# Kernel optimization log

Measured on AMD Instinct MI355X. Metric: run time of the kernel, lower is better.

## Reference

```python
import jax, jax.numpy as jnp
import numpy as np

NV, B, E, H, LF = 32, 32768, 16, 4, 4
D = E // H
FF = LF * E
EPS = 1e-5


def _gelu(x):
    return jax.nn.gelu(x, approximate=False)


def _ln(x, g, b):
    m = x.mean(-1, keepdims=True)
    v = ((x - m) ** 2).mean(-1, keepdims=True)
    return (x - m) * jax.lax.rsqrt(v + EPS) * g + b


def _mha(q_in, kv_in, wi, bi, wo, bo):
    # torch nn.MultiheadAttention, seq-first layout (S, B, E), eval mode (no dropout)
    wq, wk, wv = jnp.split(wi, 3, axis=0)
    bq, bk, bv = jnp.split(bi, 3)
    Sq, Bn = q_in.shape[0], q_in.shape[1]
    Sk = kv_in.shape[0]
    q = (q_in @ wq.T + bq).reshape(Sq, Bn, H, D)
    k = (kv_in @ wk.T + bk).reshape(Sk, Bn, H, D)
    v = (kv_in @ wv.T + bv).reshape(Sk, Bn, H, D)
    s = jnp.einsum('qbhd,kbhd->bhqk', q, k) / jnp.sqrt(jnp.asarray(D, q.dtype))
    a = jax.nn.softmax(s, axis=-1)
    o = jnp.einsum('bhqk,kbhd->qbhd', a, v).reshape(Sq, Bn, E)
    return o @ wo.T + bo


def setup_inputs() -> dict:
    key = jax.random.key(0)
    ks = iter(jax.random.split(key, 32))
    r = lambda *shape: 0.1 * jax.random.normal(next(ks), shape, dtype=jnp.float32)
    return {
        'x': jax.random.normal(next(ks), (B, NV), dtype=jnp.float32),
        'emb_w1': r(NV, LF), 'emb_b1': r(NV, LF),            # per-feature Linear(1, LF)
        'emb_w2': r(NV, LF, E), 'emb_b2': r(NV, E),          # per-feature Linear(LF, E)
        'ln1_g': jnp.ones((E,), jnp.float32), 'ln1_b': jnp.zeros((E,), jnp.float32),
        'attn_wi': r(3 * E, E), 'attn_bi': r(3 * E),
        'attn_wo': r(E, E), 'attn_bo': r(E),
        'ln2_g': jnp.ones((E,), jnp.float32), 'ln2_b': jnp.zeros((E,), jnp.float32),
        'fc1_w': r(FF, E), 'fc1_b': r(FF),
        'fc2_w': r(E, FF), 'fc2_b': r(E),
        'cls_token': jnp.zeros((E,), jnp.float32),
        'cln1_g': jnp.ones((E,), jnp.float32), 'cln1_b': jnp.zeros((E,), jnp.float32),
        'cattn_wi': r(3 * E, E), 'cattn_bi': r(3 * E),
        'cattn_wo': r(E, E), 'cattn_bo': r(E),
        'cln2_g': jnp.ones((E,), jnp.float32), 'cln2_b': jnp.zeros((E,), jnp.float32),
        'clsfc_w': r(1, E), 'clsfc_b': r(1),
    }


def reference(x, emb_w1, emb_b1, emb_w2, emb_b2, ln1_g, ln1_b,
              attn_wi, attn_bi, attn_wo, attn_bo, ln2_g, ln2_b,
              fc1_w, fc1_b, fc2_w, fc2_b, cls_token,
              cln1_g, cln1_b, cattn_wi, cattn_bi, cattn_wo, cattn_bo,
              cln2_g, cln2_b, clsfc_w, clsfc_b):
    # --- per-feature tokenizer: batched tiny MLPs (vectorized over nvars) ---
    h = _gelu(x[:, :, None] * emb_w1[None] + emb_b1[None])          # (B, NV, LF)
    e = _gelu(jnp.einsum('bvf,vfe->bve', h, emb_w2) + emb_b2[None]) # (B, NV, E)
    t = jnp.transpose(e, (1, 0, 2))                                 # (NV, B, E) seq-first
    # --- encoder block (pre-norm) ---
    res = t
    t = _ln(t, ln1_g, ln1_b)
    t = _mha(t, t, attn_wi, attn_bi, attn_wo, attn_bo) + res
    res = t
    t = _ln(t, ln2_g, ln2_b)
    t = _gelu(t @ fc1_w.T + fc1_b) @ fc2_w.T + fc2_b
    t = t + res
    # --- class-token decoder ---
    cls = jnp.broadcast_to(cls_token, (1, t.shape[1], E))           # (1, B, E)
    u = jnp.concatenate([cls, t], axis=0)                           # (NV+1, B, E)
    un = _ln(u, cln1_g, cln1_b)
    c = _mha(cls, un, cattn_wi, cattn_bi, cattn_wo, cattn_bo) + cls # query is raw cls
    c = _ln(c, cln2_g, cln2_b)
    c = c[0]                                                        # (B, E)
    out = jax.nn.sigmoid(c @ clsfc_w.T + clsfc_b)                   # (B, 1)
    return out
```

## Files before the change

### kernel.cpp

```cpp
#include <hip/hip_runtime.h>
#include <hip/hip_bf16.h>
#include <math.h>

#define NV 32
#define E  16
#define FF 64
#define BATCH 32768
#define L2E 1.4426950408889634f

static constexpr float EPS = 1e-5f;

typedef __attribute__((ext_vector_type(8)))  short bf16x8;
typedef __attribute__((ext_vector_type(16))) float f32x16;
typedef __attribute__((ext_vector_type(4)))  unsigned u32x4;

__device__ __forceinline__ short f2bf(float f) {
    __hip_bfloat16 h = __float2bfloat16(f);
    return __builtin_bit_cast(short, h);
}
__device__ __forceinline__ unsigned pack2(float a, float b) {
    return (unsigned)(unsigned short)f2bf(a) | ((unsigned)(unsigned short)f2bf(b) << 16);
}
__device__ __forceinline__ void halfswap(unsigned &a, unsigned &b) {
    const auto r = __builtin_amdgcn_permlane32_swap(a, b, false, false);
    a = (unsigned)r[0]; b = (unsigned)r[1];
}
__device__ __forceinline__ float addxhalf(float v) {
    const unsigned u = __builtin_bit_cast(unsigned, v);
    const auto r = __builtin_amdgcn_permlane32_swap(u, u, false, false);
    return __builtin_bit_cast(float, (unsigned)r[0]) + __builtin_bit_cast(float, (unsigned)r[1]);
}
__device__ __forceinline__ int psi(int h, int i) {
    return 4 * h + (i & 3) + 8 * (i >> 2);
}
__device__ __forceinline__ float ex2(float x) { return __builtin_amdgcn_exp2f(x); }
__device__ __forceinline__ float gelu_fast(float x) {
    const float x2 = x * x;
    const float u  = x * fmaf(x2, 0.10294324f, 2.3022082f);
    return x - x * __builtin_amdgcn_rcpf(1.0f + ex2(u));
}
__device__ __forceinline__ bf16x8 pack8(const float* v) {
    bf16x8 r;
#pragma unroll
    for (int i = 0; i < 8; i++) r[i] = f2bf(v[i]);
    return r;
}
__device__ __forceinline__ float dot16(const float* __restrict__ wrow, const float* __restrict__ v) {
    float s = 0.f;
#pragma unroll
    for (int j = 0; j < 16; j++) s = fmaf(wrow[j], v[j], s);
    return s;
}

__global__ __launch_bounds__(256, 4) void event_classifier_kernel(
    const float* __restrict__ x,
    const float* __restrict__ emb_w1,
    const float* __restrict__ emb_b1,
    const float* __restrict__ emb_w2,
    const float* __restrict__ emb_b2,
    const float* __restrict__ ln1_g, const float* __restrict__ ln1_b,
    const float* __restrict__ attn_wi,
    const float* __restrict__ attn_bi,
    const float* __restrict__ attn_wo,
    const float* __restrict__ attn_bo,
    const float* __restrict__ ln2_g, const float* __restrict__ ln2_b,
    const float* __restrict__ fc1_w,
    const float* __restrict__ fc1_b,
    const float* __restrict__ fc2_w,
    const float* __restrict__ fc2_b,
    const float* __restrict__ cls_token,
    const float* __restrict__ cln1_g, const float* __restrict__ cln1_b,
    const float* __restrict__ cattn_wi,
    const float* __restrict__ cattn_bi,
    const float* __restrict__ cattn_wo,
    const float* __restrict__ cattn_bo,
    const float* __restrict__ cln2_g, const float* __restrict__ cln2_b,
    const float* __restrict__ clsfc_w,
    const float* __restrict__ clsfc_b,
    float* __restrict__ out)
{
    __shared__ alignas(16) unsigned s_frag[11][64][4];
    __shared__ alignas(16) float s_bias[8][32];
    __shared__ alignas(16) unsigned short s_vt[4][4][5][40];
    __shared__ alignas(16) float s_cls[48];
    __shared__ alignas(16) float s_cw[20];

    const int tid = threadIdx.x;
    const int l   = tid & 63;
    const int t   = l & 31;
    const int hh  = l >> 5;
    const int w   = tid >> 6;
    const int b   = blockIdx.x * 4 + w;

    for (int f0 = 0; f0 < 12; f0 += 4) {
        const int f = f0 + w;
        if (f < 11) {
            const float* W; const float* gc = nullptr;
            int stride = 16, coff = 0; bool valid = true; float rscale = 1.0f;
            switch (f) {
                case 0:  W = attn_wi;        gc = ln1_g; if (t < 16) rscale = 0.5f * L2E; break;
                case 1:  W = attn_wi + 512;  gc = ln1_g; valid = (t < 16); break;
                case 2:  W = attn_wo;        valid = (t < 16); break;
                case 3:  W = fc1_w;          gc = ln2_g; break;
                case 4:  W = fc1_w + 512;    gc = ln2_g; break;
                case 5: case 6: case 7: case 8:
                         W = fc2_w; stride = 64; coff = (f - 5) * 16; valid = (t < 16); break;
                case 9:  W = cattn_wi + 256; gc = cln1_g; break;
                default: W = cattn_wo;       valid = (t < 16); break;
            }
            unsigned d[4] = {0u, 0u, 0u, 0u};
            if (valid) {
                const float* row = W + t * stride + coff;
#pragma unroll
                for (int e2 = 0; e2 < 4; e2++) {
                    const int p0 = psi(hh, 2 * e2), p1 = psi(hh, 2 * e2 + 1);
                    const float g0 = gc ? gc[p0] : 1.0f;
                    const float g1 = gc ? gc[p1] : 1.0f;
                    d[e2] = pack2(row[p0] * g0 * rscale, row[p1] * g1 * rscale);
                }
            }
            s_frag[f][l][0] = d[0]; s_frag[f][l][1] = d[1];
            s_frag[f][l][2] = d[2]; s_frag[f][l][3] = d[3];
        }
    }
    {
        const int i = tid;
        const int mat = i >> 5, idx = i & 31, h2 = idx >> 4, r = idx & 15;
        const int p8 = psi(h2, r & 7);
        float val = 0.f;
        switch (mat) {
            case 0:
                if (r < 8) val = (attn_bi[p8] + dot16(attn_wi + p8 * 16, ln1_b)) * (0.5f * L2E);
                else       val =  attn_bi[16 + p8] + dot16(attn_wi + (16 + p8) * 16, ln1_b);
                break;
            case 1: if (r < 8) val = attn_bi[32 + p8] + dot16(attn_wi + (32 + p8) * 16, ln1_b); break;
            case 2: if (r < 8) val = attn_bo[p8]; break;
            case 3: { const int p16 = psi(h2, r); val = fc1_b[p16] + dot16(fc1_w + p16 * 16, ln2_b); } break;
            case 4: { const int p16 = psi(h2, r); val = fc1_b[32 + p16] + dot16(fc1_w + (32 + p16) * 16, ln2_b); } break;
            case 5: if (r < 8) val = fc2_b[p8]; break;
            case 6:
                if (r < 8) val = cattn_bi[16 + p8] + dot16(cattn_wi + (16 + p8) * 16, cln1_b);
                else       val = cattn_bi[32 + p8] + dot16(cattn_wi + (32 + p8) * 16, cln1_b);
                break;
            default: if (r < 8) val = cattn_bo[p8] + cls_token[p8]; break;
        }
        s_bias[mat][idx] = val;
    }
    if (tid < 16) {
        const int jp = tid;
        float cls[E];
        float m = 0.f;
#pragma unroll
        for (int j = 0; j < E; j++) { cls[j] = cls_token[j]; m += cls[j]; }
        m *= (1.0f / E);
        float var = 0.f;
#pragma unroll
        for (int j = 0; j < E; j++) { float d = cls[j] - m; var += d * d; }
        var *= (1.0f / E);
        float r = rsqrtf(var + EPS);
        float un0[E];
#pragma unroll
        for (int j = 0; j < E; j++) un0[j] = (cls[j] - m) * r * cln1_g[j] + cln1_b[j];
        float qq = cattn_bi[jp], kk = cattn_bi[16 + jp], vv2 = cattn_bi[32 + jp];
#pragma unroll
        for (int j = 0; j < E; j++) {
            qq  += cls[j] * cattn_wi[jp * E + j];
            kk  += un0[j] * cattn_wi[(16 + jp) * E + j];
            vv2 += un0[j] * cattn_wi[(32 + jp) * E + j];
        }
        s_cls[jp] = qq * (0.5f * L2E); s_cls[16 + jp] = kk; s_cls[32 + jp] = vv2;
        s_cw[jp] = cln2_g[jp] * clsfc_w[jp];
        if (jp == 0) {
            float s = clsfc_b[0];
#pragma unroll
            for (int j = 0; j < E; j++) s = fmaf(cln2_b[j], clsfc_w[j], s);
            s_cw[16] = s;
        }
    }
    __syncthreads();

#define LD4(p) (*reinterpret_cast<const float4*>(p))
#define FRAG(f) (*reinterpret_cast<const bf16x8*>(&s_frag[f][l][0]))
#define CBIAS8(mat, c) { const float4 lo_ = LD4(&s_bias[mat][hh*16]); \
                         const float4 hi_ = LD4(&s_bias[mat][hh*16+4]); \
                         c[0]=lo_.x; c[1]=lo_.y; c[2]=lo_.z; c[3]=lo_.w; \
                         c[4]=hi_.x; c[5]=hi_.y; c[6]=hi_.z; c[7]=hi_.w; \
                         c[8]=0;c[9]=0;c[10]=0;c[11]=0;c[12]=0;c[13]=0;c[14]=0;c[15]=0; }
#define CBIAS16(mat, c) { const float4 a_ = LD4(&s_bias[mat][hh*16]); \
                          const float4 b_ = LD4(&s_bias[mat][hh*16+4]); \
                          const float4 c_ = LD4(&s_bias[mat][hh*16+8]); \
                          const float4 d_ = LD4(&s_bias[mat][hh*16+12]); \
                          c[0]=a_.x;c[1]=a_.y;c[2]=a_.z;c[3]=a_.w; \
                          c[4]=b_.x;c[5]=b_.y;c[6]=b_.z;c[7]=b_.w; \
                          c[8]=c_.x;c[9]=c_.y;c[10]=c_.z;c[11]=c_.w; \
                          c[12]=d_.x;c[13]=d_.y;c[14]=d_.z;c[15]=d_.w; }

    f32x16 z16;
#pragma unroll
    for (int i = 0; i < 16; i++) z16[i] = 0.0f;

    const float xv = x[b * NV + t];
    float F[8];
    {
        const float4 w1 = LD4(emb_w1 + t * 4);
        const float4 b1 = LD4(emb_b1 + t * 4);
        float hb[4];
        hb[0] = gelu_fast(fmaf(xv, w1.x, b1.x));
        hb[1] = gelu_fast(fmaf(xv, w1.y, b1.y));
        hb[2] = gelu_fast(fmaf(xv, w1.z, b1.z));
        hb[3] = gelu_fast(fmaf(xv, w1.w, b1.w));
        float a[8];
        const float4 bA = LD4(emb_b2 + t * 16 + 4 * hh);
        const float4 bB = LD4(emb_b2 + t * 16 + 8 + 4 * hh);
        a[0]=bA.x; a[1]=bA.y; a[2]=bA.z; a[3]=bA.w;
        a[4]=bB.x; a[5]=bB.y; a[6]=bB.z; a[7]=bB.w;
#pragma unroll
        for (int f = 0; f < 4; f++) {
            const float4 wA = LD4(emb_w2 + t * 64 + f * 16 + 4 * hh);
            const float4 wB = LD4(emb_w2 + t * 64 + f * 16 + 8 + 4 * hh);
            a[0] = fmaf(hb[f], wA.x, a[0]); a[1] = fmaf(hb[f], wA.y, a[1]);
            a[2] = fmaf(hb[f], wA.z, a[2]); a[3] = fmaf(hb[f], wA.w, a[3]);
            a[4] = fmaf(hb[f], wB.x, a[4]); a[5] = fmaf(hb[f], wB.y, a[5]);
            a[6] = fmaf(hb[f], wB.z, a[6]); a[7] = fmaf(hb[f], wB.w, a[7]);
        }
#pragma unroll
        for (int r = 0; r < 8; r++) F[r] = gelu_fast(a[r]);
    }

#define LN_CANON(src, dst) { \
        float s_ = 0.f; \
        _Pragma("unroll") for (int r = 0; r < 8; r++) s_ += src[r]; \
        s_ = addxhalf(s_); \
        const float m_ = s_ * (1.0f / 16.0f); \
        float vs_ = 0.f; \
        _Pragma("unroll") for (int r = 0; r < 8; r++) { float d_ = src[r] - m_; vs_ = fmaf(d_, d_, vs_); } \
        vs_ = addxhalf(vs_); \
        const float rs_ = rsqrtf(vs_ * (1.0f / 16.0f) + EPS); \
        _Pragma("unroll") for (int r = 0; r < 8; r++) dst[r] = (src[r] - m_) * rs_; }

    float res[8];
#pragma unroll
    for (int r = 0; r < 8; r++) res[r] = F[r];
    float tn[8];
    LN_CANON(F, tn);

    const bf16x8 bt = pack8(tn);
    f32x16 cqk, cv;
    CBIAS16(0, cqk); CBIAS8(1, cv);
    const f32x16 dqk = __builtin_amdgcn_mfma_f32_32x32x16_bf16(FRAG(0), bt, cqk, 0, 0, 0);
    const f32x16 dv  = __builtin_amdgcn_mfma_f32_32x32x16_bf16(FRAG(1), bt, cv, 0, 0, 0);

    unsigned qx0 = pack2(dqk[0],  dqk[1]),  qx1 = pack2(dqk[2],  dqk[3]);
    unsigned qx2 = pack2(dqk[4],  dqk[5]),  qx3 = pack2(dqk[6],  dqk[7]);
    unsigned kx0 = pack2(dqk[8],  dqk[9]),  kx1 = pack2(dqk[10], dqk[11]);
    unsigned kx2 = pack2(dqk[12], dqk[13]), kx3 = pack2(dqk[14], dqk[15]);
    halfswap(qx0, qx1); halfswap(qx2, qx3);
    halfswap(kx0, kx1); halfswap(kx2, kx3);

    s_vt[w][hh][0][t] = (unsigned short)f2bf(dv[0]);
    s_vt[w][hh][1][t] = (unsigned short)f2bf(dv[1]);
    s_vt[w][hh][2][t] = (unsigned short)f2bf(dv[2]);
    s_vt[w][hh][3][t] = (unsigned short)f2bf(dv[3]);
    s_vt[w][hh + 2][0][t] = (unsigned short)f2bf(dv[4]);
    s_vt[w][hh + 2][1][t] = (unsigned short)f2bf(dv[5]);
    s_vt[w][hh + 2][2][t] = (unsigned short)f2bf(dv[6]);
    s_vt[w][hh + 2][3][t] = (unsigned short)f2bf(dv[7]);
    s_vt[w][hh][4][t]     = 0x3F80;
    s_vt[w][hh + 2][4][t] = 0x3F80;
    asm volatile("s_waitcnt lgkmcnt(0)" ::: "memory");
    __builtin_amdgcn_sched_barrier(0);

    const int mr = (t < 5) ? t : 0;
    unsigned um0[4], um1[4];
#pragma unroll
    for (int h = 0; h < 4; h++) {
        const unsigned qf = (h == 0) ? qx0 : (h == 1) ? qx1 : (h == 2) ? qx2 : qx3;
        const unsigned kf = (h == 0) ? kx0 : (h == 1) ? kx1 : (h == 2) ? kx2 : kx3;
        const u32x4 au = {kf, 0u, 0u, 0u};
        const u32x4 bu = {qf, 0u, 0u, 0u};
        const f32x16 S = __builtin_amdgcn_mfma_f32_32x32x16_bf16(
            __builtin_bit_cast(bf16x8, au), __builtin_bit_cast(bf16x8, bu), z16, 0, 0, 0);
        unsigned w0 = pack2(ex2(S[0]),  ex2(S[1]));
        unsigned w1 = pack2(ex2(S[2]),  ex2(S[3]));
        unsigned w2 = pack2(ex2(S[4]),  ex2(S[5]));
        unsigned w3 = pack2(ex2(S[6]),  ex2(S[7]));
        unsigned w4 = pack2(ex2(S[8]),  ex2(S[9]));
        unsigned w5 = pack2(ex2(S[10]), ex2(S[11]));
        unsigned w6 = pack2(ex2(S[12]), ex2(S[13]));
        unsigned w7 = pack2(ex2(S[14]), ex2(S[15]));
        halfswap(w0, w2); halfswap(w1, w3);
        halfswap(w4, w6); halfswap(w5, w7);
        const u32x4 b1u = {w0, w1, w2, w3};
        const u32x4 b2u = {w4, w5, w6, w7};
        const bf16x8 A1 = *reinterpret_cast<const bf16x8*>(&s_vt[w][h][mr][8 * hh]);
        const bf16x8 A2 = *reinterpret_cast<const bf16x8*>(&s_vt[w][h][mr][8 * hh + 16]);
        f32x16 R = __builtin_amdgcn_mfma_f32_32x32x16_bf16(A1, __builtin_bit_cast(bf16x8, b1u), z16, 0, 0, 0);
        R = __builtin_amdgcn_mfma_f32_32x32x16_bf16(A2, __builtin_bit_cast(bf16x8, b2u), R, 0, 0, 0);
        const unsigned ru = __builtin_bit_cast(unsigned, R[0]);
        const auto rr = __builtin_amdgcn_permlane32_swap(ru, ru, false, false);
        const float rl = __builtin_amdgcn_rcpf(__builtin_bit_cast(float, (unsigned)rr[1]));
        um0[h] = pack2(R[0] * rl, R[1] * rl);
        um1[h] = pack2(R[2] * rl, R[3] * rl);
    }
    halfswap(um0[0], um0[1]); halfswap(um1[0], um1[1]);
    halfswap(um0[2], um0[3]); halfswap(um1[2], um1[3]);
    const u32x4 bou = {um0[0], um1[0], um0[2], um1[2]};
    const bf16x8 bo = __builtin_bit_cast(bf16x8, bou);

    {
        f32x16 co; CBIAS8(2, co);
        const f32x16 dto = __builtin_amdgcn_mfma_f32_32x32x16_bf16(FRAG(2), bo, co, 0, 0, 0);
#pragma unroll
        for (int r = 0; r < 8; r++) F[r] = dto[r] + res[r];
    }

#pragma unroll
    for (int r = 0; r < 8; r++) res[r] = F[r];
    float tn2[8];
    LN_CANON(F, tn2);
    {
        const bf16x8 bt2 = pack8(tn2);
        f32x16 c1, c2;
        CBIAS16(3, c1); CBIAS16(4, c2);
        const f32x16 g1 = __builtin_amdgcn_mfma_f32_32x32x16_bf16(FRAG(3), bt2, c1, 0, 0, 0);
        const f32x16 g2 = __builtin_amdgcn_mfma_f32_32x32x16_bf16(FRAG(4), bt2, c2, 0, 0, 0);
        float gva[16], gvb[16];
#pragma unroll
        for (int r = 0; r < 16; r++) gva[r] = gelu_fast(g1[r]);
#pragma unroll
        for (int r = 0; r < 16; r++) gvb[r] = gelu_fast(g2[r]);
        const bf16x8 pk0 = pack8(gva), pk1 = pack8(gva + 8);
        const bf16x8 pk2 = pack8(gvb), pk3 = pack8(gvb + 8);
        f32x16 acc; CBIAS8(5, acc);
        acc = __builtin_amdgcn_mfma_f32_32x32x16_bf16(FRAG(5), pk0, acc, 0, 0, 0);
        acc = __builtin_amdgcn_mfma_f32_32x32x16_bf16(FRAG(6), pk1, acc, 0, 0, 0);
        acc = __builtin_amdgcn_mfma_f32_32x32x16_bf16(FRAG(7), pk2, acc, 0, 0, 0);
        acc = __builtin_amdgcn_mfma_f32_32x32x16_bf16(FRAG(8), pk3, acc, 0, 0, 0);
#pragma unroll
        for (int r = 0; r < 8; r++) F[r] = acc[r] + res[r];
    }

    float tn3[8];
    LN_CANON(F, tn3);
    const bf16x8 bt3 = pack8(tn3);
    f32x16 ckv; CBIAS16(6, ckv);
    const f32x16 dkv = __builtin_amdgcn_mfma_f32_32x32x16_bf16(FRAG(9), bt3, ckv, 0, 0, 0);

    const float4 qcA = LD4(s_cls + 4 * hh);
    const float4 qcB = LD4(s_cls + 8 + 4 * hh);
    const float sA2 = fmaf(qcA.x, dkv[0], fmaf(qcA.y, dkv[1], fmaf(qcA.z, dkv[2], qcA.w * dkv[3])));
    const float sB2 = fmaf(qcB.x, dkv[4], fmaf(qcB.y, dkv[5], fmaf(qcB.z, dkv[6], qcB.w * dkv[7])));
    const float pA2 = ex2(sA2), pB2 = ex2(sB2);
    const float4 k0A = LD4(s_cls + 16 + 4 * hh);
    const float4 k0B = LD4(s_cls + 16 + 8 + 4 * hh);
    const float s0A = fmaf(qcA.x, k0A.x, fmaf(qcA.y, k0A.y, fmaf(qcA.z, k0A.z, qcA.w * k0A.w)));
    const float s0B = fmaf(qcB.x, k0B.x, fmaf(qcB.y, k0B.y, fmaf(qcB.z, k0B.z, qcB.w * k0B.w)));
    const float p0A = ex2(s0A), p0B = ex2(s0B);

    float lA2 = pA2, lB2 = pB2;
    float oc[8];
    oc[0] = pA2 * dkv[8];  oc[1] = pA2 * dkv[9];  oc[2] = pA2 * dkv[10]; oc[3] = pA2 * dkv[11];
    oc[4] = pB2 * dkv[12]; oc[5] = pB2 * dkv[13]; oc[6] = pB2 * dkv[14]; oc[7] = pB2 * dkv[15];
#pragma unroll
    for (int mask = 1; mask <= 16; mask <<= 1) {
        lA2 += __shfl_xor(lA2, mask);
        lB2 += __shfl_xor(lB2, mask);
#pragma unroll
        for (int r = 0; r < 8; r++) oc[r] += __shfl_xor(oc[r], mask);
    }
    {
        const float4 v0A = LD4(s_cls + 32 + 4 * hh);
        const float4 v0B = LD4(s_cls + 32 + 8 + 4 * hh);
        const float rA2 = __builtin_amdgcn_rcpf(lA2 + p0A);
        const float rB2 = __builtin_amdgcn_rcpf(lB2 + p0B);
        oc[0] = (oc[0] + p0A * v0A.x) * rA2; oc[1] = (oc[1] + p0A * v0A.y) * rA2;
        oc[2] = (oc[2] + p0A * v0A.z) * rA2; oc[3] = (oc[3] + p0A * v0A.w) * rA2;
        oc[4] = (oc[4] + p0B * v0B.x) * rB2; oc[5] = (oc[5] + p0B * v0B.y) * rB2;
        oc[6] = (oc[6] + p0B * v0B.z) * rB2; oc[7] = (oc[7] + p0B * v0B.w) * rB2;
    }

    float c8[8];
    {
        const bf16x8 boc = pack8(oc);
        f32x16 cc; CBIAS8(7, cc);
        const f32x16 dc = __builtin_amdgcn_mfma_f32_32x32x16_bf16(FRAG(10), boc, cc, 0, 0, 0);
#pragma unroll
        for (int r = 0; r < 8; r++) c8[r] = dc[r];
    }
    {
        float s = 0.f;
#pragma unroll
        for (int r = 0; r < 8; r++) s += c8[r];
        s = addxhalf(s);
        const float m = s * (1.0f / 16.0f);
        float vs = 0.f;
#pragma unroll
        for (int r = 0; r < 8; r++) { const float d = c8[r] - m; vs = fmaf(d, d, vs); }
        vs = addxhalf(vs);
        const float rstd = rsqrtf(vs * (1.0f / 16.0f) + EPS);
        const float4 wA = LD4(s_cw + 4 * hh), wB = LD4(s_cw + 8 + 4 * hh);
        float zp = 0.f;
        zp = fmaf((c8[0] - m) * rstd, wA.x, zp);
        zp = fmaf((c8[1] - m) * rstd, wA.y, zp);
        zp = fmaf((c8[2] - m) * rstd, wA.z, zp);
        zp = fmaf((c8[3] - m) * rstd, wA.w, zp);
        zp = fmaf((c8[4] - m) * rstd, wB.x, zp);
        zp = fmaf((c8[5] - m) * rstd, wB.y, zp);
        zp = fmaf((c8[6] - m) * rstd, wB.z, zp);
        zp = fmaf((c8[7] - m) * rstd, wB.w, zp);
        const float z = addxhalf(zp) + s_cw[16];
        const float sig = __builtin_amdgcn_rcpf(1.0f + ex2(-L2E * z));
        if (l == 0) out[b] = sig;
    }
}

extern "C" void kernel_launch(void* const* d_in, const int* in_sizes, int n_in,
                              void* d_out, int out_size, void* d_ws, size_t ws_size,
                              hipStream_t stream) {
    const float* x        = (const float*)d_in[0];
    const float* emb_w1   = (const float*)d_in[1];
    const float* emb_b1   = (const float*)d_in[2];
    const float* emb_w2   = (const float*)d_in[3];
    const float* emb_b2   = (const float*)d_in[4];
    const float* ln1_g    = (const float*)d_in[5];
    const float* ln1_b    = (const float*)d_in[6];
    const float* attn_wi  = (const float*)d_in[7];
    const float* attn_bi  = (const float*)d_in[8];
    const float* attn_wo  = (const float*)d_in[9];
    const float* attn_bo  = (const float*)d_in[10];
    const float* ln2_g    = (const float*)d_in[11];
    const float* ln2_b    = (const float*)d_in[12];
    const float* fc1_w    = (const float*)d_in[13];
    const float* fc1_b    = (const float*)d_in[14];
    const float* fc2_w    = (const float*)d_in[15];
    const float* fc2_b    = (const float*)d_in[16];
    const float* cls_tok  = (const float*)d_in[17];
    const float* cln1_g   = (const float*)d_in[18];
    const float* cln1_b   = (const float*)d_in[19];
    const float* cattn_wi = (const float*)d_in[20];
    const float* cattn_bi = (const float*)d_in[21];
    const float* cattn_wo = (const float*)d_in[22];
    const float* cattn_bo = (const float*)d_in[23];
    const float* cln2_g   = (const float*)d_in[24];
    const float* cln2_b   = (const float*)d_in[25];
    const float* clsfc_w  = (const float*)d_in[26];
    const float* clsfc_b  = (const float*)d_in[27];
    float* out = (float*)d_out;

    const int grid = BATCH / 4;
    event_classifier_kernel<<<grid, 256, 0, stream>>>(
        x, emb_w1, emb_b1, emb_w2, emb_b2, ln1_g, ln1_b,
        attn_wi, attn_bi, attn_wo, attn_bo, ln2_g, ln2_b,
        fc1_w, fc1_b, fc2_w, fc2_b, cls_tok,
        cln1_g, cln1_b, cattn_wi, cattn_bi, cattn_wo, cattn_bo,
        cln2_g, cln2_b, clsfc_w, clsfc_b, out);
}
```

Measured before the change: 97.04 us.

## Raise occupancy, use DPP reductions, vectorize weight loads, fold LN into FMA

Raises the launch-bounds occupancy hint from 4 to 8 blocks per SM, forcing tighter register allocation. The cross-lane sums in the class-token attention now use DPP row_shr adds plus one shuffle instead of butterfly __shfl_xor loops. Weight-fragment and dot16 setup loads use float4, and layernorm normalization is folded into a single fma with a precomputed -mean*rstd. Capping registers may cause spills, and the DPP reduction only leaves the full sum in some lanes, which may break lanes that read oc later.

Measured after the change: 100.2 us. 3.3% more time.

```diff
diff --git a/kernel.cpp b/kernel.cpp
--- a/kernel.cpp
+++ b/kernel.cpp
@@ -14,6 +14,8 @@
 typedef __attribute__((ext_vector_type(16))) float f32x16;
 typedef __attribute__((ext_vector_type(4)))  unsigned u32x4;
 
+#define LD4(p) (*reinterpret_cast<const float4*>(p))
+
 __device__ __forceinline__ short f2bf(float f) {
     __hip_bfloat16 h = __float2bfloat16(f);
     return __builtin_bit_cast(short, h);
@@ -29,6 +31,18 @@
     const unsigned u = __builtin_bit_cast(unsigned, v);
     const auto r = __builtin_amdgcn_permlane32_swap(u, u, false, false);
     return __builtin_bit_cast(float, (unsigned)r[0]) + __builtin_bit_cast(float, (unsigned)r[1]);
+}
+template <int CTRL>
+__device__ __forceinline__ float dpp_add(float v) {
+    const int s = __builtin_amdgcn_update_dpp(0, __builtin_bit_cast(int, v), CTRL, 0xF, 0xF, true);
+    return v + __builtin_bit_cast(float, s);
+}
+__device__ __forceinline__ float sum32(float v) {
+    v = dpp_add<0x121>(v);
+    v = dpp_add<0x122>(v);
+    v = dpp_add<0x124>(v);
+    v = dpp_add<0x128>(v);
+    return v + __shfl_xor(v, 16);
 }
 __device__ __forceinline__ int psi(int h, int i) {
     return 4 * h + (i & 3) + 8 * (i >> 2);
@@ -48,11 +62,15 @@
 __device__ __forceinline__ float dot16(const float* __restrict__ wrow, const float* __restrict__ v) {
     float s = 0.f;
 #pragma unroll
-    for (int j = 0; j < 16; j++) s = fmaf(wrow[j], v[j], s);
+    for (int j = 0; j < 4; j++) {
+        const float4 a = LD4(wrow + 4 * j);
+        const float4 c = LD4(v + 4 * j);
+        s = fmaf(a.x, c.x, fmaf(a.y, c.y, fmaf(a.z, c.z, fmaf(a.w, c.w, s))));
+    }
     return s;
 }
 
-__global__ __launch_bounds__(256, 4) void event_classifier_kernel(
+__global__ __launch_bounds__(256, 8) void event_classifier_kernel(
     const float* __restrict__ x,
     const float* __restrict__ emb_w1,
     const float* __restrict__ emb_b1,
@@ -110,14 +128,19 @@
             }
             unsigned d[4] = {0u, 0u, 0u, 0u};
             if (valid) {
-                const float* row = W + t * stride + coff;
-#pragma unroll
-                for (int e2 = 0; e2 < 4; e2++) {
-                    const int p0 = psi(hh, 2 * e2), p1 = psi(hh, 2 * e2 + 1);
-                    const float g0 = gc ? gc[p0] : 1.0f;
-                    const float g1 = gc ? gc[p1] : 1.0f;
-                    d[e2] = pack2(row[p0] * g0 * rscale, row[p1] * g1 * rscale);
+                const float* row = W + t * stride + coff + 4 * hh;
+                float4 r0 = LD4(row);
+                float4 r1 = LD4(row + 8);
+                if (gc) {
+                    const float4 g0 = LD4(gc + 4 * hh);
+                    const float4 g1 = LD4(gc + 8 + 4 * hh);
+                    r0.x *= g0.x; r0.y *= g0.y; r0.z *= g0.z; r0.w *= g0.w;
+                    r1.x *= g1.x; r1.y *= g1.y; r1.z *= g1.z; r1.w *= g1.w;
                 }
+                r0.x *= rscale; r0.y *= rscale; r0.z *= rscale; r0.w *= rscale;
+                r1.x *= rscale; r1.y *= rscale; r1.z *= rscale; r1.w *= rscale;
+                d[0] = pack2(r0.x, r0.y); d[1] = pack2(r0.z, r0.w);
+                d[2] = pack2(r1.x, r1.y); d[3] = pack2(r1.z, r1.w);
             }
             s_frag[f][l][0] = d[0]; s_frag[f][l][1] = d[1];
             s_frag[f][l][2] = d[2]; s_frag[f][l][3] = d[3];
@@ -179,7 +202,6 @@
     }
     __syncthreads();
 
-#define LD4(p) (*reinterpret_cast<const float4*>(p))
 #define FRAG(f) (*reinterpret_cast<const bf16x8*>(&s_frag[f][l][0]))
 #define CBIAS8(mat, c) { const float4 lo_ = LD4(&s_bias[mat][hh*16]); \
                          const float4 hi_ = LD4(&s_bias[mat][hh*16+4]); \
@@ -236,7 +258,8 @@
         _Pragma("unroll") for (int r = 0; r < 8; r++) { float d_ = src[r] - m_; vs_ = fmaf(d_, d_, vs_); } \
         vs_ = addxhalf(vs_); \
         const float rs_ = rsqrtf(vs_ * (1.0f / 16.0f) + EPS); \
-        _Pragma("unroll") for (int r = 0; r < 8; r++) dst[r] = (src[r] - m_) * rs_; }
+        const float nm_ = -m_ * rs_; \
+        _Pragma("unroll") for (int r = 0; r < 8; r++) dst[r] = fmaf(src[r], rs_, nm_); }
 
     float res[8];
 #pragma unroll
@@ -357,17 +380,12 @@
     const float s0B = fmaf(qcB.x, k0B.x, fmaf(qcB.y, k0B.y, fmaf(qcB.z, k0B.z, qcB.w * k0B.w)));
     const float p0A = ex2(s0A), p0B = ex2(s0B);
 
-    float lA2 = pA2, lB2 = pB2;
+    float lA2 = sum32(pA2), lB2 = sum32(pB2);
     float oc[8];
-    oc[0] = pA2 * dkv[8];  oc[1] = pA2 * dkv[9];  oc[2] = pA2 * dkv[10]; oc[3] = pA2 * dkv[11];
-    oc[4] = pB2 * dkv[12]; oc[5] = pB2 * dkv[13]; oc[6] = pB2 * dkv[14]; oc[7] = pB2 * dkv[15];
-#pragma unroll
-    for (int mask = 1; mask <= 16; mask <<= 1) {
-        lA2 += __shfl_xor(lA2, mask);
-        lB2 += __shfl_xor(lB2, mask);
-#pragma unroll
-        for (int r = 0; r < 8; r++) oc[r] += __shfl_xor(oc[r], mask);
-    }
+    oc[0] = sum32(pA2 * dkv[8]);  oc[1] = sum32(pA2 * dkv[9]);
+    oc[2] = sum32(pA2 * dkv[10]); oc[3] = sum32(pA2 * dkv[11]);
+    oc[4] = sum32(pB2 * dkv[12]); oc[5] = sum32(pB2 * dkv[13]);
+    oc[6] = sum32(pB2 * dkv[14]); oc[7] = sum32(pB2 * dkv[15]);
     {
         const float4 v0A = LD4(s_cls + 32 + 4 * hh);
         const float4 v0B = LD4(s_cls + 32 + 8 + 4 * hh);
@@ -398,16 +416,17 @@
         for (int r = 0; r < 8; r++) { const float d = c8[r] - m; vs = fmaf(d, d, vs); }
         vs = addxhalf(vs);
         const float rstd = rsqrtf(vs * (1.0f / 16.0f) + EPS);
+        const float nm = -m * rstd;
         const float4 wA = LD4(s_cw + 4 * hh), wB = LD4(s_cw + 8 + 4 * hh);
         float zp = 0.f;
-        zp = fmaf((c8[0] - m) * rstd, wA.x, zp);
-        zp = fmaf((c8[1] - m) * rstd, wA.y, zp);
-        zp = fmaf((c8[2] - m) * rstd, wA.z, zp);
-        zp = fmaf((c8[3] - m) * rstd, wA.w, zp);
-        zp = fmaf((c8[4] - m) * rstd, wB.x, zp);
-        zp = fmaf((c8[5] - m) * rstd, wB.y, zp);
-        zp = fmaf((c8[6] - m) * rstd, wB.z, zp);
-        zp = fmaf((c8[7] - m) * rstd, wB.w, zp);
+        zp = fmaf(fmaf(c8[0], rstd, nm), wA.x, zp);
+        zp = fmaf(fmaf(c8[1], rstd, nm), wA.y, zp);
+        zp = fmaf(fmaf(c8[2], rstd, nm), wA.z, zp);
+        zp = fmaf(fmaf(c8[3], rstd, nm), wA.w, zp);
+        zp = fmaf(fmaf(c8[4], rstd, nm), wB.x, zp);
+        zp = fmaf(fmaf(c8[5], rstd, nm), wB.y, zp);
+        zp = fmaf(fmaf(c8[6], rstd, nm), wB.z, zp);
+        zp = fmaf(fmaf(c8[7], rstd, nm), wB.w, zp);
         const float z = addxhalf(zp) + s_cw[16];
         const float sig = __builtin_amdgcn_rcpf(1.0f + ex2(-L2E * z));
         if (l == 0) out[b] = sig;
```
